# Performance work log

Measured on AMD Instinct MI355X. Metric: run time of the kernel, lower is better.

## Reference

```python
import jax, jax.numpy as jnp
import numpy as np

B, NQ, NK = 4, 2048, 2048
D_MODEL, H, DK, DV, M = 512, 8, 64, 64, 40


def setup_inputs() -> dict:
    key = jax.random.key(0)
    ks = jax.random.split(key, 12)
    s = 0.02  # param init scale (stand-in for xavier)
    return {
        "queries": jax.random.normal(ks[0], (B, NQ, D_MODEL), jnp.float32),
        "keys": jax.random.normal(ks[1], (B, NK, D_MODEL), jnp.float32),
        "values": jax.random.normal(ks[2], (B, NK, D_MODEL), jnp.float32),
        "attention_weights": jax.random.uniform(ks[3], (B, H, NQ, NK), jnp.float32),
        "attention_mask": jax.random.randint(ks[4], (B, H, NQ, NK), 0, 2) == 1,
        "Wq": jax.random.normal(ks[5], (D_MODEL, H * DK), jnp.float32) * s,
        "bq": jnp.zeros((H * DK,), jnp.float32),
        "Wk": jax.random.normal(ks[6], (D_MODEL, H * DK), jnp.float32) * s,
        "bk": jnp.zeros((H * DK,), jnp.float32),
        "Wv": jax.random.normal(ks[7], (D_MODEL, H * DV), jnp.float32) * s,
        "bv": jnp.zeros((H * DV,), jnp.float32),
        "Wo": jax.random.normal(ks[8], (H * DV, D_MODEL), jnp.float32) * s,
        "bo": jnp.zeros((D_MODEL,), jnp.float32),
        "m_k": jax.random.normal(ks[9], (1, M, H * DK), jnp.float32) * s,
        "m_v": jax.random.normal(ks[10], (1, M, H * DV), jnp.float32) * s,
    }


def reference(queries, keys, values, attention_weights, attention_mask,
              Wq, bq, Wk, bk, Wv, bv, Wo, bo, m_k, m_v):
    b, nq, _ = queries.shape
    nk = keys.shape[1]
    # learned memory slots, scaled and broadcast over batch
    mk = jnp.sqrt(jnp.float32(DK)) * jnp.broadcast_to(m_k, (b, M, H * DK))
    mv = jnp.sqrt(jnp.float32(M)) * jnp.broadcast_to(m_v, (b, M, H * DV))
    q = (queries @ Wq + bq).reshape(b, nq, H, DK).transpose(0, 2, 1, 3)      # (b,h,nq,dk)
    k = jnp.concatenate([keys @ Wk + bk, mk], axis=1)
    k = k.reshape(b, nk + M, H, DK).transpose(0, 2, 3, 1)                     # (b,h,dk,nk+m)
    v = jnp.concatenate([values @ Wv + bv, mv], axis=1)
    v = v.reshape(b, nk + M, H, DV).transpose(0, 2, 1, 3)                     # (b,h,nk+m,dv)
    att = jnp.matmul(q, k) / jnp.sqrt(jnp.float32(DK))                        # (b,h,nq,nk+m)
    att_x = att[..., :nk] * attention_weights
    att_x = jnp.where(attention_mask, -jnp.inf, att_x)
    att = jnp.concatenate([att_x, att[..., nk:]], axis=-1)
    att = jax.nn.softmax(att, axis=-1)
    out = jnp.matmul(att, v).transpose(0, 2, 1, 3).reshape(b, nq, H * DV)
    return out @ Wo + bo
```

## Files before the change

### kernel.cpp

```cpp
#include <hip/hip_runtime.h>
#include <hip/hip_bf16.h>
#include <cstdint>
#include <cstddef>

typedef __bf16 bf16_t;
typedef __bf16 bf16x8 __attribute__((ext_vector_type(8)));
typedef __bf16 bf16x4 __attribute__((ext_vector_type(4)));
typedef float  f32x4  __attribute__((ext_vector_type(4)));

#define B_    4
#define NQ_   2048
#define NK_   2048
#define H_    8
#define MSL_  40
#define NKP_  2112
#define SCL2  0.18033688011112042f

#define GLOAD_LDS16(GP, LP)                                                        \
    __builtin_amdgcn_global_load_lds(                                              \
        (const __attribute__((address_space(1))) unsigned int*)(GP),               \
        (__attribute__((address_space(3))) unsigned int*)(LP), 16, 0, 0)

__global__ void detect_mask(const unsigned int* __restrict__ m, int* __restrict__ flag)
{
    __shared__ int found;
    if (threadIdx.x == 0) found = 0;
    __syncthreads();
    unsigned int acc = 0;
    for (int i = threadIdx.x; i < 65536; i += 256)
        acc |= (m[i] & 0xFFFFFF00u);
    if (acc) found = 1;
    __syncthreads();
    if (threadIdx.x == 0) *flag = found;
}

__global__ void transpose_convert4(const float* __restrict__ s0, const float* __restrict__ s1,
                                   const float* __restrict__ s2, const float* __restrict__ s3,
                                   bf16_t* __restrict__ d0, bf16_t* __restrict__ d1,
                                   bf16_t* __restrict__ d2, bf16_t* __restrict__ d3)
{
    const float* src; bf16_t* dst;
    switch (blockIdx.z) {
        case 0:  src = s0; dst = d0; break;
        case 1:  src = s1; dst = d1; break;
        case 2:  src = s2; dst = d2; break;
        default: src = s3; dst = d3; break;
    }
    __shared__ float t[32][33];
    int x  = blockIdx.x * 32 + threadIdx.x;
    int y0 = blockIdx.y * 32 + threadIdx.y;
#pragma unroll
    for (int i = 0; i < 32; i += 8)
        t[threadIdx.y + i][threadIdx.x] = src[(size_t)(y0 + i) * 512 + x];
    __syncthreads();
    int ox  = blockIdx.y * 32 + threadIdx.x;
    int oy0 = blockIdx.x * 32 + threadIdx.y;
#pragma unroll
    for (int i = 0; i < 32; i += 8)
        dst[(size_t)(oy0 + i) * 512 + ox] = (bf16_t)t[threadIdx.x][threadIdx.y + i];
}

__global__ void memfill(const float* __restrict__ m_k, const float* __restrict__ m_v,
                        bf16_t* __restrict__ Kbf, bf16_t* __restrict__ Vt)
{
    int tid = blockIdx.x * 256 + threadIdx.x;
    if (tid < 4 * 64 * 512) {
        int c  = tid & 511;
        int mi = (tid >> 9) & 63;
        int b  = tid >> 15;
        float v = (mi < MSL_) ? 8.0f * m_k[mi * 512 + c] : 0.0f;
        Kbf[((size_t)b * NKP_ + NK_ + mi) * 512 + c] = (bf16_t)v;
    } else {
        int t  = tid - 4 * 64 * 512;
        int mi = t & 63;
        int dv = (t >> 6) & 63;
        int h  = (t >> 12) & 7;
        int b  = t >> 15;
        float v = (mi < MSL_) ? 6.324555320336759f * m_v[mi * 512 + h * 64 + dv] : 0.0f;
        Vt[(((size_t)b * H_ + h) * 64 + dv) * NKP_ + NK_ + mi] = (bf16_t)v;
    }
}

template<int EPI, bool AF32>
__global__ __launch_bounds__(256) void gemm_bt(
    const void* __restrict__ Av, const bf16_t* __restrict__ BT,
    const float* __restrict__ bias, void* __restrict__ dstv, int dstBS)
{
    __shared__ bf16_t As[128][72];
    __shared__ bf16_t Bs[128][72];

    const int tid = threadIdx.x;
    const int w = tid >> 6, l = tid & 63, lg = l >> 4, lr = l & 15;
    const int wr = w >> 1, wc = w & 1;
    const int blockM = blockIdx.x * 128, blockN = blockIdx.y * 128;

    f32x4 acc[4][4];
    const f32x4 zv = {0.f, 0.f, 0.f, 0.f};
#pragma unroll
    for (int i = 0; i < 4; i++)
#pragma unroll
        for (int j = 0; j < 4; j++) acc[i][j] = zv;

    const int ar = tid >> 1;
    const int ac = (tid & 1) * 32;

    for (int k0 = 0; k0 < 512; k0 += 64) {
        if (k0) __syncthreads();
        if constexpr (AF32) {
            const float* arow = (const float*)Av + (size_t)(blockM + ar) * 512 + k0 + ac;
#pragma unroll
            for (int i = 0; i < 8; i++) {
                float4 v = ((const float4*)arow)[i];
                bf16x4 pk = {(bf16_t)v.x, (bf16_t)v.y, (bf16_t)v.z, (bf16_t)v.w};
                *(bf16x4*)&As[ar][ac + i * 4] = pk;
            }
        } else {
            const bf16_t* arow = (const bf16_t*)Av + (size_t)(blockM + ar) * 512 + k0 + ac;
#pragma unroll
            for (int i = 0; i < 4; i++)
                *(uint4*)&As[ar][ac + i * 8] = ((const uint4*)arow)[i];
        }
        {
            const bf16_t* brow = BT + (size_t)(blockN + ar) * 512 + k0 + ac;
#pragma unroll
            for (int i = 0; i < 4; i++)
                *(uint4*)&Bs[ar][ac + i * 8] = ((const uint4*)brow)[i];
        }
        __syncthreads();
#pragma unroll
        for (int ks = 0; ks < 2; ks++) {
            bf16x8 af[4], bfr[4];
#pragma unroll
            for (int mi = 0; mi < 4; mi++)
                af[mi] = *(const bf16x8*)&As[wr * 64 + mi * 16 + lr][ks * 32 + lg * 8];
#pragma unroll
            for (int ni = 0; ni < 4; ni++)
                bfr[ni] = *(const bf16x8*)&Bs[wc * 64 + ni * 16 + lr][ks * 32 + lg * 8];
#pragma unroll
            for (int mi = 0; mi < 4; mi++)
#pragma unroll
                for (int ni = 0; ni < 4; ni++)
                    acc[mi][ni] = __builtin_amdgcn_mfma_f32_16x16x32_bf16(af[mi], bfr[ni], acc[mi][ni], 0, 0, 0);
        }
    }

    const int colbase = blockN + wc * 64;
    float bias_v[4];
#pragma unroll
    for (int ni = 0; ni < 4; ni++) bias_v[ni] = bias[colbase + ni * 16 + lr];

#pragma unroll
    for (int mi = 0; mi < 4; mi++) {
        const int r0 = blockM + wr * 64 + mi * 16 + lg * 4;
#pragma unroll
        for (int ni = 0; ni < 4; ni++) {
            const int c = colbase + ni * 16 + lr;
            f32x4 v = acc[mi][ni];
            if constexpr (EPI == 2) {
                float* dst = (float*)dstv;
#pragma unroll
                for (int j = 0; j < 4; j++)
                    dst[(size_t)(r0 + j) * 512 + c] = v[j] + bias_v[ni];
            } else if constexpr (EPI == 0) {
                bf16_t* dst = (bf16_t*)dstv;
#pragma unroll
                for (int j = 0; j < 4; j++) {
                    int rr = r0 + j;
                    int bb = rr >> 11, nn = rr & 2047;
                    dst[((size_t)bb * dstBS + nn) * 512 + c] = (bf16_t)(v[j] + bias_v[ni]);
                }
            } else {
                bf16_t* dst = (bf16_t*)dstv;
                int bb = r0 >> 11, n0 = r0 & 2047;
                int hh = c >> 6, dv = c & 63;
                bf16x4 pk;
#pragma unroll
                for (int j = 0; j < 4; j++) pk[j] = (bf16_t)(v[j] + bias_v[ni]);
                *(bf16x4*)(dst + (((size_t)bb * H_ + hh) * 64 + dv) * NKP_ + n0) = pk;
            }
        }
    }
}

template<bool BYTEM>
__global__ __launch_bounds__(256) void attn_fused(
    const bf16_t* __restrict__ Qbf, const bf16_t* __restrict__ Kbf,
    const bf16_t* __restrict__ Vt, const float* __restrict__ attw,
    const void* __restrict__ maskv, const int* __restrict__ mflag,
    bf16_t* __restrict__ Obuf)
{
    if ((*mflag != 0) != BYTEM) return;

    __shared__ bf16_t Ks[2][64][64];
    __shared__ bf16_t Vs[2][64][64];
    __shared__ bf16_t Pl[4][1024];

    const int tid = threadIdx.x;
    const int wv = tid >> 6, l = tid & 63, lg = l >> 4, lr = l & 15;
    const int qt = blockIdx.x, h = blockIdx.y, b = blockIdx.z;
    const int q0w = qt * 64 + wv * 16;
    bf16_t* Pw = &Pl[wv][0];

    const size_t bh = (size_t)(b * H_ + h);
    const float* wbase = attw + bh * (size_t)NQ_ * NK_;
    const unsigned char* mb8 = (const unsigned char*)maskv + bh * (size_t)NQ_ * NK_;
    const int* mb32 = (const int*)maskv + bh * (size_t)NQ_ * NK_;
    const char* kbase8 = (const char*)(Kbf + (size_t)b * NKP_ * 512 + h * 64);
    const char* vbase8 = (const char*)(Vt + bh * 64 * (size_t)NKP_);

    bf16x8 qf0 = *(const bf16x8*)&Qbf[((size_t)b * NQ_ + q0w + lr) * 512 + h * 64 + lg * 8];
    bf16x8 qf1 = *(const bf16x8*)&Qbf[((size_t)b * NQ_ + q0w + lr) * 512 + h * 64 + 32 + lg * 8];

    const f32x4 zv = {0.f, 0.f, 0.f, 0.f};
    f32x4 oacc[4];
#pragma unroll
    for (int i = 0; i < 4; i++) oacc[i] = zv;
    float mrun = -INFINITY, lsum = 0.f;
    f32x4 sA[4];

    f32x4 wA[4], wB[4];
    unsigned mA[4], mB[4];
    unsigned miA[16], miB[16];

    const int srow = l >> 3;
    const int scsw = ((l & 7) ^ (srow & 7)) * 16;

#define STAGE(BUF, KCB) do {                                                      \
    _Pragma("unroll") for (int pi_ = 0; pi_ < 2; pi_++) {                         \
        const int p_ = wv * 2 + pi_;                                              \
        const int r_ = p_ * 8 + srow;                                             \
        GLOAD_LDS16(kbase8 + (size_t)((KCB) + r_) * 1024 + scsw,                  \
                    (char*)&Ks[BUF][0][0] + p_ * 1024);                           \
        GLOAD_LDS16(vbase8 + (size_t)r_ * 4224 + (size_t)(KCB) * 2 + scsw,        \
                    (char*)&Vs[BUF][0][0] + p_ * 1024);                           \
    }                                                                             \
} while (0)

#define PREFETCH(KT, WB_, MB_, MIB_) do {                                         \
    const float* wp_ = wbase + (size_t)(q0w + lr) * NK_ + (KT) * 64 + lg * 4;     \
    _Pragma("unroll") for (int n_ = 0; n_ < 4; n_++)                              \
        WB_[n_] = *(const f32x4*)(wp_ + n_ * 16);                                 \
    if constexpr (BYTEM) {                                                        \
        const unsigned char* mp_ = mb8 + (size_t)(q0w + lr) * NK_ + (KT) * 64 + lg * 4; \
        _Pragma("unroll") for (int n_ = 0; n_ < 4; n_++)                          \
            MB_[n_] = *(const unsigned*)(mp_ + n_ * 16);                          \
    } else {                                                                      \
        const int* mp_ = mb32 + (size_t)(q0w + lr) * NK_ + (KT) * 64 + lg * 4;    \
        _Pragma("unroll") for (int n_ = 0; n_ < 4; n_++) {                        \
            uint4 t_ = *(const uint4*)(mp_ + n_ * 16);                            \
            MIB_[n_ * 4 + 0] = t_.x; MIB_[n_ * 4 + 1] = t_.y;                     \
            MIB_[n_ * 4 + 2] = t_.z; MIB_[n_ * 4 + 3] = t_.w; }                   \
    }                                                                             \
} while (0)

#define QKT_LDS(BC) do {                                                          \
    const int sw_ = (lg ^ (lr & 7)) * 8;                                          \
    _Pragma("unroll") for (int n_ = 0; n_ < 4; n_++) {                            \
        const int kr_ = n_ * 16 + lr;                                             \
        f32x4 a_ = zv;                                                            \
        a_ = __builtin_amdgcn_mfma_f32_16x16x32_bf16(*(const bf16x8*)&Ks[BC][kr_][sw_], qf0, a_, 0, 0, 0); \
        a_ = __builtin_amdgcn_mfma_f32_16x16x32_bf16(*(const bf16x8*)&Ks[BC][kr_][sw_ ^ 32], qf1, a_, 0, 0, 0); \
        sA[n_] = a_;                                                              \
    }                                                                             \
} while (0)

#define APPLY(WB_, MB_, MIB_) do {                                                \
    _Pragma("unroll") for (int n_ = 0; n_ < 4; n_++)                              \
    _Pragma("unroll") for (int j_ = 0; j_ < 4; j_++) {                            \
        bool mk_;                                                                 \
        if constexpr (BYTEM) mk_ = ((MB_[n_] >> (8 * j_)) & 0xffu) != 0;          \
        else                 mk_ = (MIB_[n_ * 4 + j_] != 0);                      \
        sA[n_][j_] = mk_ ? -1e30f : sA[n_][j_] * SCL2 * WB_[n_][j_];              \
    }                                                                             \
} while (0)

#define SMPV(BC) do {                                                             \
    float tm_ = sA[0][0];                                                         \
    _Pragma("unroll") for (int n_ = 0; n_ < 4; n_++)                              \
    _Pragma("unroll") for (int j_ = 0; j_ < 4; j_++)                              \
        tm_ = fmaxf(tm_, sA[n_][j_]);                                             \
    tm_ = fmaxf(tm_, __shfl_xor(tm_, 16));                                        \
    tm_ = fmaxf(tm_, __shfl_xor(tm_, 32));                                        \
    float mnew_ = fmaxf(mrun, tm_);                                               \
    float sc_ = exp2f(mrun - mnew_);                                              \
    mrun = mnew_;                                                                 \
    float ts_ = 0.f;                                                              \
    _Pragma("unroll") for (int n_ = 0; n_ < 4; n_++)                              \
    _Pragma("unroll") for (int j_ = 0; j_ < 4; j_++) {                            \
        float p_ = exp2f(sA[n_][j_] - mnew_);                                     \
        sA[n_][j_] = p_; ts_ += p_;                                               \
    }                                                                             \
    ts_ += __shfl_xor(ts_, 16);                                                   \
    ts_ += __shfl_xor(ts_, 32);                                                   \
    lsum = lsum * sc_ + ts_;                                                      \
    _Pragma("unroll") for (int n2_ = 0; n2_ < 4; n2_++) oacc[n2_] *= sc_;         \
    _Pragma("unroll") for (int n_ = 0; n_ < 4; n_++) {                            \
        int c_ = n_ * 2 + (lg >> 1);                                              \
        int qp_ = (lr + 4 * c_) & 15;                                             \
        bf16x4 pk_ = {(bf16_t)sA[n_][0], (bf16_t)sA[n_][1],                       \
                      (bf16_t)sA[n_][2], (bf16_t)sA[n_][3]};                      \
        *(bf16x4*)&Pw[c_ * 128 + qp_ * 8 + (lg & 1) * 4] = pk_;                   \
    }                                                                             \
    bf16x8 pf0_ = *(const bf16x8*)&Pw[lg * 128 + ((lr + 4 * lg) & 15) * 8];       \
    bf16x8 pf1_ = *(const bf16x8*)&Pw[(4 + lg) * 128 + ((lr + 4 * (4 + lg)) & 15) * 8]; \
    const int vsw_ = (lg ^ (lr & 7)) * 8;                                         \
    _Pragma("unroll") for (int n2_ = 0; n2_ < 4; n2_++) {                         \
        const int vr_ = n2_ * 16 + lr;                                            \
        oacc[n2_] = __builtin_amdgcn_mfma_f32_16x16x32_bf16(*(const bf16x8*)&Vs[BC][vr_][vsw_], pf0_, oacc[n2_], 0, 0, 0); \
        oacc[n2_] = __builtin_amdgcn_mfma_f32_16x16x32_bf16(*(const bf16x8*)&Vs[BC][vr_][vsw_ ^ 32], pf1_, oacc[n2_], 0, 0, 0); \
    }                                                                             \
} while (0)

#define WAITBAR(WCNT) do {                                                        \
    asm volatile("s_waitcnt vmcnt(" WCNT ")" ::: "memory");                       \
    __builtin_amdgcn_s_barrier();                                                 \
    __builtin_amdgcn_sched_barrier(0);                                            \
} while (0)

#define BODY(KT, BC, BN, WC_, MC_, MIC_) do {                                     \
    WAITBAR("8");                                                                 \
    if ((KT) < 31) { STAGE(BN, ((KT) + 1) * 64); }                                \
    __builtin_amdgcn_sched_barrier(0);                                            \
    QKT_LDS(BC);                                                                  \
    APPLY(WC_, MC_, MIC_);                                                        \
    if ((KT) < 30) { PREFETCH((KT) + 2, WC_, MC_, MIC_); }                        \
    SMPV(BC);                                                                     \
} while (0)

    STAGE(0, 2048);
    __builtin_amdgcn_sched_barrier(0);
    PREFETCH(0, wA, mA, miA);

    {
        WAITBAR("8");
        STAGE(1, 0);
        __builtin_amdgcn_sched_barrier(0);
        QKT_LDS(0);
#pragma unroll
        for (int n_ = 0; n_ < 4; n_++)
#pragma unroll
            for (int j_ = 0; j_ < 4; j_++) {
                int kloc = n_ * 16 + lg * 4 + j_;
                sA[n_][j_] = (kloc >= MSL_) ? -1e30f : sA[n_][j_] * SCL2;
            }
        PREFETCH(1, wB, mB, miB);
        SMPV(0);
    }

    for (int kt = 0; kt < 30; kt += 2) {
        BODY(kt,     1, 0, wA, mA, miA);
        BODY(kt + 1, 0, 1, wB, mB, miB);
    }
    BODY(30, 1, 0, wA, mA, miA);
    {
        WAITBAR("0");
        QKT_LDS(0);
        APPLY(wB, mB, miB);
        SMPV(0);
    }

    float invl = 1.0f / lsum;
#pragma unroll
    for (int n2 = 0; n2 < 4; n2++) {
        bf16x4 ov = {(bf16_t)(oacc[n2][0] * invl), (bf16_t)(oacc[n2][1] * invl),
                     (bf16_t)(oacc[n2][2] * invl), (bf16_t)(oacc[n2][3] * invl)};
        *(bf16x4*)&Obuf[((size_t)b * NQ_ + q0w + lr) * 512 + h * 64 + n2 * 16 + lg * 4] = ov;
    }

#undef STAGE
#undef PREFETCH
#undef QKT_LDS
#undef APPLY
#undef SMPV
#undef WAITBAR
#undef BODY
}

extern "C" void kernel_launch(void* const* d_in, const int* in_sizes, int n_in,
                              void* d_out, int out_size, void* d_ws, size_t ws_size,
                              hipStream_t stream)
{
    const float* queries = (const float*)d_in[0];
    const float* keys    = (const float*)d_in[1];
    const float* values  = (const float*)d_in[2];
    const float* attw    = (const float*)d_in[3];
    const void*  maskv   = d_in[4];
    const float* Wq = (const float*)d_in[5];
    const float* bq = (const float*)d_in[6];
    const float* Wk = (const float*)d_in[7];
    const float* bk = (const float*)d_in[8];
    const float* Wv = (const float*)d_in[9];
    const float* bv = (const float*)d_in[10];
    const float* Wo = (const float*)d_in[11];
    const float* bo = (const float*)d_in[12];
    const float* m_k = (const float*)d_in[13];
    const float* m_v = (const float*)d_in[14];

    char* ws = (char*)d_ws;
    bf16_t* WqT  = (bf16_t*)(ws + 0);
    bf16_t* WkT  = (bf16_t*)(ws + 524288);
    bf16_t* WvT  = (bf16_t*)(ws + 1048576);
    bf16_t* WoT  = (bf16_t*)(ws + 1572864);
    bf16_t* Qbf  = (bf16_t*)(ws + 2097152);
    bf16_t* Kbf  = (bf16_t*)(ws + 10485760);
    bf16_t* Vt   = (bf16_t*)(ws + 19136512);
    bf16_t* Obuf = (bf16_t*)(ws + 27787264);
    int*    mflag = (int*)(ws + 36175872);

    detect_mask<<<1, 256, 0, stream>>>((const unsigned int*)maskv, mflag);
    transpose_convert4<<<dim3(16, 16, 4), dim3(32, 8), 0, stream>>>(
        Wq, Wk, Wv, Wo, WqT, WkT, WvT, WoT);
    memfill<<<1024, 256, 0, stream>>>(m_k, m_v, Kbf, Vt);

    gemm_bt<0, true><<<dim3(64, 4), 256, 0, stream>>>(queries, WqT, bq, Qbf, 2048);
    gemm_bt<0, true><<<dim3(64, 4), 256, 0, stream>>>(keys,    WkT, bk, Kbf, NKP_);
    gemm_bt<1, true><<<dim3(64, 4), 256, 0, stream>>>(values,  WvT, bv, Vt, 0);

    attn_fused<true><<<dim3(32, H_, B_), 256, 0, stream>>>(Qbf, Kbf, Vt, attw, maskv, mflag, Obuf);
    attn_fused<false><<<dim3(32, H_, B_), 256, 0, stream>>>(Qbf, Kbf, Vt, attw, maskv, mflag, Obuf);

    gemm_bt<2, false><<<dim3(64, 4), 256, 0, stream>>>(Obuf, WoT, bo, d_out, 0);
    (void)in_sizes; (void)n_in; (void)out_size; (void)ws_size;
}
```

Measured before the change: 370.3 us.

## Batch QKV projections into one launch, enlarge attention tiles, fold scale into Q

Merges the three Q/K/V projection GEMMs into a single launch selected by blockIdx.z, which removes two launches and lets their blocks run together. The attention kernel moves to 512 threads covering 128 queries per block, so each K/V tile staged in LDS serves twice as many query rows and each wave now stages one slice instead of two. The softmax scale is folded into the Q projection epilogue, removing a multiply per score in the attention loop. The trade-offs are a runtime epilogue switch in the GEMM, Q rounded to bf16 after scaling, and higher per-block register and LDS use that may reduce occupancy.

After: 344.0 us. -7.1%, faster.

```diff
diff --git a/kernel.cpp b/kernel.cpp
--- a/kernel.cpp
+++ b/kernel.cpp
@@ -81,14 +81,13 @@
     }
 }
 
-template<int EPI, bool AF32>
-__global__ __launch_bounds__(256) void gemm_bt(
+template<bool AF32>
+__device__ __forceinline__ void gemm_core(
+    bf16_t (*As)[72], bf16_t (*Bs)[72],
     const void* __restrict__ Av, const bf16_t* __restrict__ BT,
-    const float* __restrict__ bias, void* __restrict__ dstv, int dstBS)
-{
-    __shared__ bf16_t As[128][72];
-    __shared__ bf16_t Bs[128][72];
-
+    const float* __restrict__ bias, void* __restrict__ dstv,
+    int dstBS, int epi, float scale)
+{
     const int tid = threadIdx.x;
     const int w = tid >> 6, l = tid & 63, lg = l >> 4, lr = l & 15;
     const int wr = w >> 1, wc = w & 1;
@@ -156,18 +155,18 @@
         for (int ni = 0; ni < 4; ni++) {
             const int c = colbase + ni * 16 + lr;
             f32x4 v = acc[mi][ni];
-            if constexpr (EPI == 2) {
+            if (epi == 2) {
                 float* dst = (float*)dstv;
 #pragma unroll
                 for (int j = 0; j < 4; j++)
-                    dst[(size_t)(r0 + j) * 512 + c] = v[j] + bias_v[ni];
-            } else if constexpr (EPI == 0) {
+                    dst[(size_t)(r0 + j) * 512 + c] = (v[j] + bias_v[ni]) * scale;
+            } else if (epi == 0) {
                 bf16_t* dst = (bf16_t*)dstv;
 #pragma unroll
                 for (int j = 0; j < 4; j++) {
                     int rr = r0 + j;
                     int bb = rr >> 11, nn = rr & 2047;
-                    dst[((size_t)bb * dstBS + nn) * 512 + c] = (bf16_t)(v[j] + bias_v[ni]);
+                    dst[((size_t)bb * dstBS + nn) * 512 + c] = (bf16_t)((v[j] + bias_v[ni]) * scale);
                 }
             } else {
                 bf16_t* dst = (bf16_t*)dstv;
@@ -175,15 +174,42 @@
                 int hh = c >> 6, dv = c & 63;
                 bf16x4 pk;
 #pragma unroll
-                for (int j = 0; j < 4; j++) pk[j] = (bf16_t)(v[j] + bias_v[ni]);
+                for (int j = 0; j < 4; j++) pk[j] = (bf16_t)((v[j] + bias_v[ni]) * scale);
                 *(bf16x4*)(dst + (((size_t)bb * H_ + hh) * 64 + dv) * NKP_ + n0) = pk;
             }
         }
     }
 }
 
+__global__ __launch_bounds__(256) void gemm_qkv(
+    const float* __restrict__ q, const float* __restrict__ k, const float* __restrict__ v,
+    const bf16_t* __restrict__ WqT, const bf16_t* __restrict__ WkT, const bf16_t* __restrict__ WvT,
+    const float* __restrict__ bq, const float* __restrict__ bk, const float* __restrict__ bv,
+    bf16_t* __restrict__ Qbf, bf16_t* __restrict__ Kbf, bf16_t* __restrict__ Vt)
+{
+    __shared__ bf16_t As[128][72];
+    __shared__ bf16_t Bs[128][72];
+    const void* Av; const bf16_t* BT; const float* bias; void* dst;
+    int dstBS, epi; float scale = 1.0f;
+    switch (blockIdx.z) {
+        case 0:  Av = q; BT = WqT; bias = bq; dst = Qbf; dstBS = 2048; epi = 0; scale = SCL2; break;
+        case 1:  Av = k; BT = WkT; bias = bk; dst = Kbf; dstBS = NKP_; epi = 0; break;
+        default: Av = v; BT = WvT; bias = bv; dst = Vt;  dstBS = 0;    epi = 1; break;
+    }
+    gemm_core<true>(As, Bs, Av, BT, bias, dst, dstBS, epi, scale);
+}
+
+__global__ __launch_bounds__(256) void gemm_fin(
+    const bf16_t* __restrict__ Obuf, const bf16_t* __restrict__ WoT,
+    const float* __restrict__ bo, float* __restrict__ out)
+{
+    __shared__ bf16_t As[128][72];
+    __shared__ bf16_t Bs[128][72];
+    gemm_core<false>(As, Bs, Obuf, WoT, bo, out, 0, 2, 1.0f);
+}
+
 template<bool BYTEM>
-__global__ __launch_bounds__(256) void attn_fused(
+__global__ __launch_bounds__(512) void attn_fused(
     const bf16_t* __restrict__ Qbf, const bf16_t* __restrict__ Kbf,
     const bf16_t* __restrict__ Vt, const float* __restrict__ attw,
     const void* __restrict__ maskv, const int* __restrict__ mflag,
@@ -193,12 +219,12 @@
 
     __shared__ bf16_t Ks[2][64][64];
     __shared__ bf16_t Vs[2][64][64];
-    __shared__ bf16_t Pl[4][1024];
+    __shared__ bf16_t Pl[8][1024];
 
     const int tid = threadIdx.x;
     const int wv = tid >> 6, l = tid & 63, lg = l >> 4, lr = l & 15;
     const int qt = blockIdx.x, h = blockIdx.y, b = blockIdx.z;
-    const int q0w = qt * 64 + wv * 16;
+    const int q0w = qt * 128 + wv * 16;
     bf16_t* Pw = &Pl[wv][0];
 
     const size_t bh = (size_t)(b * H_ + h);
@@ -226,14 +252,11 @@
     const int scsw = ((l & 7) ^ (srow & 7)) * 16;
 
 #define STAGE(BUF, KCB) do {                                                      \
-    _Pragma("unroll") for (int pi_ = 0; pi_ < 2; pi_++) {                         \
-        const int p_ = wv * 2 + pi_;                                              \
-        const int r_ = p_ * 8 + srow;                                             \
-        GLOAD_LDS16(kbase8 + (size_t)((KCB) + r_) * 1024 + scsw,                  \
-                    (char*)&Ks[BUF][0][0] + p_ * 1024);                           \
-        GLOAD_LDS16(vbase8 + (size_t)r_ * 4224 + (size_t)(KCB) * 2 + scsw,        \
-                    (char*)&Vs[BUF][0][0] + p_ * 1024);                           \
-    }                                                                             \
+    const int r_ = wv * 8 + srow;                                                 \
+    GLOAD_LDS16(kbase8 + (size_t)((KCB) + r_) * 1024 + scsw,                      \
+                (char*)&Ks[BUF][0][0] + wv * 1024);                               \
+    GLOAD_LDS16(vbase8 + (size_t)r_ * 4224 + (size_t)(KCB) * 2 + scsw,            \
+                (char*)&Vs[BUF][0][0] + wv * 1024);                               \
 } while (0)
 
 #define PREFETCH(KT, WB_, MB_, MIB_) do {                                         \
@@ -270,7 +293,7 @@
         bool mk_;                                                                 \
         if constexpr (BYTEM) mk_ = ((MB_[n_] >> (8 * j_)) & 0xffu) != 0;          \
         else                 mk_ = (MIB_[n_ * 4 + j_] != 0);                      \
-        sA[n_][j_] = mk_ ? -1e30f : sA[n_][j_] * SCL2 * WB_[n_][j_];              \
+        sA[n_][j_] = mk_ ? -1e30f : sA[n_][j_] * WB_[n_][j_];                     \
     }                                                                             \
 } while (0)
 
@@ -341,7 +364,7 @@
 #pragma unroll
             for (int j_ = 0; j_ < 4; j_++) {
                 int kloc = n_ * 16 + lg * 4 + j_;
-                sA[n_][j_] = (kloc >= MSL_) ? -1e30f : sA[n_][j_] * SCL2;
+                sA[n_][j_] = (kloc >= MSL_) ? -1e30f : sA[n_][j_];
             }
         PREFETCH(1, wB, mB, miB);
         SMPV(0);
@@ -412,13 +435,12 @@
         Wq, Wk, Wv, Wo, WqT, WkT, WvT, WoT);
     memfill<<<1024, 256, 0, stream>>>(m_k, m_v, Kbf, Vt);
 
-    gemm_bt<0, true><<<dim3(64, 4), 256, 0, stream>>>(queries, WqT, bq, Qbf, 2048);
-    gemm_bt<0, true><<<dim3(64, 4), 256, 0, stream>>>(keys,    WkT, bk, Kbf, NKP_);
-    gemm_bt<1, true><<<dim3(64, 4), 256, 0, stream>>>(values,  WvT, bv, Vt, 0);
-
-    attn_fused<true><<<dim3(32, H_, B_), 256, 0, stream>>>(Qbf, Kbf, Vt, attw, maskv, mflag, Obuf);
-    attn_fused<false><<<dim3(32, H_, B_), 256, 0, stream>>>(Qbf, Kbf, Vt, attw, maskv, mflag, Obuf);
-
-    gemm_bt<2, false><<<dim3(64, 4), 256, 0, stream>>>(Obuf, WoT, bo, d_out, 0);
+    gemm_qkv<<<dim3(64, 4, 3), 256, 0, stream>>>(
+        queries, keys, values, WqT, WkT, WvT, bq, bk, bv, Qbf, Kbf, Vt);
+
+    attn_fused<true><<<dim3(16, H_, B_), 512, 0, stream>>>(Qbf, Kbf, Vt, attw, maskv, mflag, Obuf);
+    attn_fused<false><<<dim3(16, H_, B_), 512, 0, stream>>>(Qbf, Kbf, Vt, attw, maskv, mflag, Obuf);
+
+    gemm_fin<<<dim3(64, 4), 256, 0, stream>>>(Obuf, WoT, bo, (float*)d_out);
     (void)in_sizes; (void)n_in; (void)out_size; (void)ws_size;
 }
```
